# Optimization experiments

Measured on AMD Instinct MI355X. Metric: run time of the kernel, lower is better.

The kernel has to match this reference:

```python
import jax, jax.numpy as jnp
import numpy as np

B, G = 64, 48            # events, grid side -> N = B*G*G nodes
N = B * G * G
DIMS = [128, 102, 73, 44, 16]   # channel schedule from GraphZ defaults
KERN = 3                 # GMM kernels on the conv layer
MAXV = 1.0               # Cartesian(max_value=neighbors=1)


def _build_graph():
    # 3x3 window graph (radius 1, self loops) per event, as in window_edges
    ix, iy = np.meshgrid(np.arange(G), np.arange(G), indexing='ij')
    ix, iy = ix.ravel(), iy.ravel()
    srcs, tgts = [], []
    for dx in (-1, 0, 1):
        for dy in (-1, 0, 1):
            jx, jy = ix + dx, iy + dy
            m = (jx >= 0) & (jx < G) & (jy >= 0) & (jy < G)
            srcs.append(jx[m] * G + jy[m])
            tgts.append(ix[m] * G + iy[m])
    src, tgt = np.concatenate(srcs), np.concatenate(tgts)
    base = (np.arange(B) * G * G)[:, None]
    ei = np.stack([(base + src[None]).ravel(), (base + tgt[None]).ravel()])
    pos = np.stack([np.tile(ix, B).astype(np.float32),
                    np.tile(iy, B).astype(np.float32),
                    np.repeat(np.arange(B), G * G).astype(np.float32)], axis=1)
    return ei.astype(np.int32), pos


def setup_inputs() -> dict:
    key = jax.random.key(0)
    ks = jax.random.split(key, 16)
    ei, pos = _build_graph()
    inp = {
        'x': jax.random.normal(ks[0], (N, DIMS[0]), jnp.float32),
        'pos': jnp.asarray(pos),
        'edge_index': jnp.asarray(ei),
    }
    # pointwise layer 0: 128->102 (+BN)
    inp['w0'] = jax.random.normal(ks[1], (DIMS[0], DIMS[1]), jnp.float32) * (1.0 / np.sqrt(DIMS[0]))
    inp['b0'] = jnp.zeros((DIMS[1],), jnp.float32)
    inp['gamma0'] = jnp.ones((DIMS[1],), jnp.float32)
    inp['beta0'] = jnp.zeros((DIMS[1],), jnp.float32)
    # pointwise layer 1: 102->73 (+BN)
    inp['w1'] = jax.random.normal(ks[2], (DIMS[1], DIMS[2]), jnp.float32) * (1.0 / np.sqrt(DIMS[1]))
    inp['b1'] = jnp.zeros((DIMS[2],), jnp.float32)
    inp['gamma1'] = jnp.ones((DIMS[2],), jnp.float32)
    inp['beta1'] = jnp.zeros((DIMS[2],), jnp.float32)
    # GMM conv layer 2: 73->44, 3 gaussian kernels (+BN)
    inp['w2'] = jax.random.normal(ks[3], (DIMS[2], DIMS[3]), jnp.float32) * (1.0 / np.sqrt(DIMS[2]))
    inp['g2'] = jax.random.normal(ks[4], (DIMS[2], KERN * DIMS[3]), jnp.float32) * (1.0 / np.sqrt(DIMS[2]))
    inp['mu2'] = jax.random.uniform(ks[5], (KERN, 2), jnp.float32)
    inp['sigma2'] = jax.random.uniform(ks[6], (KERN, 2), jnp.float32) + 0.5
    inp['b2'] = jnp.zeros((DIMS[3],), jnp.float32)
    inp['gamma2'] = jnp.ones((DIMS[3],), jnp.float32)
    inp['beta2'] = jnp.zeros((DIMS[3],), jnp.float32)
    # pointwise layer 3: 44->16
    inp['w3'] = jax.random.normal(ks[7], (DIMS[3], DIMS[4]), jnp.float32) * (1.0 / np.sqrt(DIMS[3]))
    inp['b3'] = jnp.zeros((DIMS[4],), jnp.float32)
    return inp


def _bn(x, gamma, beta):
    # BatchNorm1d training forward: biased batch stats over the node dim
    m = jnp.mean(x, axis=0)
    v = jnp.mean((x - m) ** 2, axis=0)
    return (x - m) * jax.lax.rsqrt(v + 1e-5) * gamma + beta


def _gmm_conv(x, ei, ea, g, mu, sigma, w_root, b, n):
    # PyG GMMConv (separate_gaussians=False, aggr='mean', root_weight, bias)
    E = ea.shape[0]
    kk = mu.shape[0]
    out = w_root.shape[1]
    xj = (x @ g)[ei[0]].reshape(E, kk, out)                 # gather transformed src feats
    gauss = jnp.exp(jnp.sum(-0.5 * (ea[:, None, :] - mu[None]) ** 2
                            / (1e-15 + sigma[None] ** 2), axis=-1))  # [E, K]
    msg = jnp.einsum('eko,ek->eo', xj, gauss)               # [E, out]
    s = jax.ops.segment_sum(msg, ei[1], num_segments=n)     # scatter-add to targets
    c = jax.ops.segment_sum(jnp.ones((E,), x.dtype), ei[1], num_segments=n)
    return s / jnp.maximum(c, 1.0)[:, None] + x @ w_root + b


def reference(x, pos, edge_index, w0, b0, gamma0, beta0, w1, b1, gamma1, beta1,
              w2, g2, mu2, sigma2, b2, gamma2, beta2, w3, b3):
    n = x.shape[0]
    pos2 = pos[:, :2]
    # Cartesian(max_value=1, norm=True): pseudo coords in [0, 1]
    ea = (pos2[edge_index[0]] - pos2[edge_index[1]]) / (2.0 * MAXV) + 0.5
    # layers 0,1: knn_graph(k=0) -> empty edge set -> GMMConv = root Linear + bias
    h = _bn(x @ w0 + b0, gamma0, beta0)
    h = _bn(h @ w1 + b1, gamma1, beta1)
    # layer 2: window-edge GMMConv with 3 gaussian kernels
    h = _bn(_gmm_conv(h, edge_index, ea, g2, mu2, sigma2, w2, b2, n), gamma2, beta2)
    # layer 3: pointwise, no norm
    return h @ w3 + b3
```

## Files before the change

kernel.cpp:

```cpp
#include <hip/hip_runtime.h>

#define GRIDW 48
#define NNODES 147456
#define NTILES 2304
#define GB 512
#define NSH 8
#define SHS 128

typedef __attribute__((ext_vector_type(8))) short short8;
typedef __attribute__((ext_vector_type(4))) float f32x4;

__device__ inline unsigned short f2bf(float f) {
    union { float f; unsigned u; } v; v.f = f;
    unsigned r = v.u + 0x7FFFu + ((v.u >> 16) & 1u);
    return (unsigned short)(r >> 16);
}
__device__ inline float bf2f(unsigned short h) {
    union { unsigned u; float f; } v; v.u = ((unsigned)h) << 16;
    return v.f;
}

__global__ void prep(const float* __restrict__ w0, const float* __restrict__ b0,
                     const float* __restrict__ w1, const float* __restrict__ b1,
                     const float* __restrict__ g2, const float* __restrict__ w2,
                     const float* __restrict__ b2, const float* __restrict__ w3,
                     const float* __restrict__ b3,
                     unsigned short* __restrict__ wt0, unsigned short* __restrict__ wt1,
                     unsigned short* __restrict__ wt2, unsigned short* __restrict__ wt3,
                     float* __restrict__ biasf0, float* __restrict__ biasf1,
                     float* __restrict__ biasf2, float* __restrict__ biasf3,
                     float* __restrict__ statz) {
    int id = blockIdx.x * 256 + threadIdx.x;
    if (id < 14336) {
        int col = id >> 7, k = id & 127;
        wt0[id] = (col < 102) ? f2bf(w0[k * 102 + col]) : (unsigned short)0;
    } else if (id < 24576) {
        int e = id - 14336; int col = e >> 7, k = e & 127;
        wt1[e] = (col < 73 && k < 102) ? f2bf(w1[k * 73 + col]) : (unsigned short)0;
    } else if (id < 41472) {
        int e = id - 24576; int col = e / 96, k = e - (e / 96) * 96;
        unsigned short v = 0;
        if (k < 73) v = (col < 132) ? f2bf(g2[k * 132 + col]) : f2bf(w2[k * 44 + (col - 132)]);
        wt2[e] = v;
    } else if (id < 42496) {
        int e = id - 41472; int col = e >> 6, k = e & 63;
        wt3[e] = (k < 44) ? f2bf(w3[k * 16 + col]) : (unsigned short)0;
    } else if (id < 42608) { int c = id - 42496; biasf0[c] = (c < 102) ? b0[c] : 0.f; }
    else if (id < 42688) { int c = id - 42608; biasf1[c] = (c < 73) ? b1[c] : 0.f; }
    else if (id < 42864) { int c = id - 42688; biasf2[c] = (c < 132) ? 0.f : b2[c - 132]; }
    else if (id < 42880) { int c = id - 42864; biasf3[c] = b3[c]; }
    else if (id < 49024) { statz[id - 42880] = 0.f; }
}

template<int K, int KP, int MP, int MOUT, int PREVM, int BNSRC,
         bool STATS, bool OUTBF, bool ABF16>
__global__ __launch_bounds__(256) void gemm_p(
    const void* __restrict__ Ain, const unsigned short* __restrict__ WT,
    const float* __restrict__ biasf,
    const float* __restrict__ q0, const float* __restrict__ q1,
    const float* __restrict__ q2, const float* __restrict__ q3,
    float invN, void* __restrict__ Yout,
    float* __restrict__ sumO, float* __restrict__ ssO)
{
    constexpr int KS = KP + 8;
    constexpr int NCF = MP / 16;
    constexpr int UPR = ABF16 ? (K / 8) : (K / 4);
    constexpr int TOT = 64 * UPR;
    constexpr int NLD = (TOT + 255) / 256;
    __shared__ __align__(16) unsigned short As[2][64 * KS];
    __shared__ __align__(16) unsigned short Bs[MP * KS];
    __shared__ float bnA[KP], bnB[KP];

    const int tid = threadIdx.x;
    const int lane = tid & 63, wv = tid >> 6, qd = lane >> 4, lc = lane & 15;

    if (BNSRC == 1) {
        if (tid < KP) {
            float a = 0.f, b = 0.f;
            if (tid < PREVM) {
                float s0 = 0.f, s1 = 0.f;
#pragma unroll
                for (int sh = 0; sh < NSH; ++sh) {
                    s0 += q0[sh * SHS + tid];
                    s1 += q1[sh * SHS + tid];
                }
                float m = s0 * invN;
                float v = s1 * invN - m * m;
                float sc = q2[tid] * rsqrtf(v + 1e-5f);
                a = sc; b = q3[tid] - m * sc;
            }
            bnA[tid] = a; bnB[tid] = b;
        }
    }
    for (int g = tid; g < MP * (KP / 8); g += 256) {
        int col = g / (KP / 8), u = g - col * (KP / 8);
        *(uint4*)&Bs[col * KS + u * 8] = *(const uint4*)&WT[(size_t)col * KP + u * 8];
    }
    if constexpr (KP > K) {
        constexpr int PADU = (KP - K) / 2;
        for (int g = tid; g < 64 * PADU; g += 256) {
            int row = g / PADU, u = g - row * PADU;
            *(unsigned*)&As[0][row * KS + K + u * 2] = 0u;
            *(unsigned*)&As[1][row * KS + K + u * 2] = 0u;
        }
    }

    float bvr[NCF];
#pragma unroll
    for (int cf = 0; cf < NCF; ++cf) bvr[cf] = biasf[cf * 16 + lc];

    float cs[NCF], cq[NCF];
    if (STATS) {
#pragma unroll
        for (int cf = 0; cf < NCF; ++cf) { cs[cf] = 0.f; cq[cf] = 0.f; }
    }

    uint4 pfb[NLD];
    float4 pff[NLD];

    int t = blockIdx.x;
#pragma unroll
    for (int i = 0; i < NLD; ++i) {
        int g = tid + 256 * i;
        if (g < TOT) {
            if constexpr (ABF16)
                pfb[i] = *(const uint4*)((const unsigned short*)Ain + (size_t)t * 64 * K + g * 8);
            else
                pff[i] = *(const float4*)((const float*)Ain + (size_t)t * 64 * K + g * 4);
        }
    }
    __syncthreads();

    int buf = 0;
    for (; t < NTILES; t += GB) {
#pragma unroll
        for (int i = 0; i < NLD; ++i) {
            int g = tid + 256 * i;
            if (g < TOT) {
                int row = g / UPR, u = g - row * UPR;
                if constexpr (ABF16) {
                    uint4 w = pfb[i];
                    if (BNSRC != 0) {
                        unsigned* wp = (unsigned*)&w;
#pragma unroll
                        for (int pp = 0; pp < 4; ++pp) {
                            int kk = u * 8 + 2 * pp;
                            float lo = bf2f((unsigned short)(wp[pp] & 0xFFFFu)) * bnA[kk] + bnB[kk];
                            float hi = bf2f((unsigned short)(wp[pp] >> 16)) * bnA[kk + 1] + bnB[kk + 1];
                            wp[pp] = (unsigned)f2bf(lo) | ((unsigned)f2bf(hi) << 16);
                        }
                    }
                    *(uint4*)&As[buf][row * KS + u * 8] = w;
                } else {
                    float4 v = pff[i];
                    if (BNSRC != 0) {
                        int kk = u * 4;
                        v.x = v.x * bnA[kk] + bnB[kk];
                        v.y = v.y * bnA[kk + 1] + bnB[kk + 1];
                        v.z = v.z * bnA[kk + 2] + bnB[kk + 2];
                        v.w = v.w * bnA[kk + 3] + bnB[kk + 3];
                    }
                    unsigned lo = (unsigned)f2bf(v.x) | ((unsigned)f2bf(v.y) << 16);
                    unsigned hi = (unsigned)f2bf(v.z) | ((unsigned)f2bf(v.w) << 16);
                    *(uint2*)&As[buf][row * KS + u * 4] = make_uint2(lo, hi);
                }
            }
        }
        int t2 = t + GB;
        if (t2 < NTILES) {
#pragma unroll
            for (int i = 0; i < NLD; ++i) {
                int g = tid + 256 * i;
                if (g < TOT) {
                    if constexpr (ABF16)
                        pfb[i] = *(const uint4*)((const unsigned short*)Ain + (size_t)t2 * 64 * K + g * 8);
                    else
                        pff[i] = *(const float4*)((const float*)Ain + (size_t)t2 * 64 * K + g * 4);
                }
            }
        }
        __syncthreads();

        f32x4 acc[NCF];
#pragma unroll
        for (int cf = 0; cf < NCF; ++cf) acc[cf] = (f32x4){0.f, 0.f, 0.f, 0.f};
#pragma unroll
        for (int kt = 0; kt < KP / 32; ++kt) {
            const int kb = kt * 32 + qd * 8;
            short8 a = *(const short8*)&As[buf][(wv * 16 + lc) * KS + kb];
#pragma unroll
            for (int cf = 0; cf < NCF; ++cf) {
                short8 b = *(const short8*)&Bs[(cf * 16 + lc) * KS + kb];
                acc[cf] = __builtin_amdgcn_mfma_f32_16x16x32_bf16(a, b, acc[cf], 0, 0, 0);
            }
        }
#pragma unroll
        for (int cf = 0; cf < NCF; ++cf) {
            const int col = cf * 16 + lc;
            const float bv = bvr[cf];
#pragma unroll
            for (int rr = 0; rr < 4; ++rr) {
                float v = acc[cf][rr] + bv;
                int row = t * 64 + wv * 16 + qd * 4 + rr;
                if (OUTBF) ((unsigned short*)Yout)[(size_t)row * MP + col] = f2bf(v);
                else       ((float*)Yout)[(size_t)row * MP + col] = v;
                if (STATS) { cs[cf] += v; cq[cf] += v * v; }
            }
        }
        buf ^= 1;
    }

    if (STATS) {
        __syncthreads();
        float* red = (float*)As;
        float* redq = red + 4 * MP;
#pragma unroll
        for (int cf = 0; cf < NCF; ++cf) {
            float s = cs[cf], qq = cq[cf];
            s += __shfl_down(s, 32, 64); s += __shfl_down(s, 16, 64);
            qq += __shfl_down(qq, 32, 64); qq += __shfl_down(qq, 16, 64);
            if (lane < 16) {
                red[wv * MP + cf * 16 + lane] = s;
                redq[wv * MP + cf * 16 + lane] = qq;
            }
        }
        __syncthreads();
        if (tid < MOUT) {
            float s = red[tid] + red[MP + tid] + red[2 * MP + tid] + red[3 * MP + tid];
            float qq = redq[tid] + redq[MP + tid] + redq[2 * MP + tid] + redq[3 * MP + tid];
            const int sh = blockIdx.x & (NSH - 1);
            atomicAdd(&sumO[sh * SHS + tid], s);
            atomicAdd(&ssO[sh * SHS + tid], qq);
        }
    }
}

__device__ __forceinline__ void load_u(const unsigned short* __restrict__ TR,
                                       int b, int jx, int iy, int c0,
                                       const float (*gy)[3], float (&u)[12]) {
#pragma unroll
    for (int j = 0; j < 12; ++j) u[j] = 0.f;
    if (jx < 0 || jx >= GRIDW) return;
    const unsigned short* rowp = TR + (size_t)(b * 2304 + jx * 48) * 176;
#pragma unroll
    for (int dy = -1; dy <= 1; ++dy) {
        int jy = iy + dy;
        if (jy < 0 || jy >= GRIDW) continue;
        const unsigned short* np = rowp + (size_t)jy * 176 + c0;
#pragma unroll
        for (int k = 0; k < 3; ++k) {
            uint2 v = *(const uint2*)(np + k * 44);
            float g = gy[dy + 1][k];
            u[k * 4 + 0] += g * bf2f((unsigned short)(v.x & 0xFFFFu));
            u[k * 4 + 1] += g * bf2f((unsigned short)(v.x >> 16));
            u[k * 4 + 2] += g * bf2f((unsigned short)(v.y & 0xFFFFu));
            u[k * 4 + 3] += g * bf2f((unsigned short)(v.y >> 16));
        }
    }
}

__global__ __launch_bounds__(256) void gmm_stencil(
    const unsigned short* __restrict__ TR, unsigned short* __restrict__ C,
    const float* __restrict__ mu, const float* __restrict__ sigma,
    float* __restrict__ sum2, float* __restrict__ ss2)
{
    __shared__ float gx[3][3], gy[3][3];
    __shared__ float red[88];
    const int tid = threadIdx.x;
    if (tid < 88) red[tid] = 0.f;
    if (tid < 18) {
        int d = (tid / 3) % 3, k = tid % 3;
        bool isy = tid >= 9;
        float e = 0.5f * (float)(d - 1) + 0.5f;
        float mm = mu[k * 2 + (isy ? 1 : 0)];
        float sg = sigma[k * 2 + (isy ? 1 : 0)];
        float v = expf(-0.5f * (e - mm) * (e - mm) / (1e-15f + sg * sg));
        if (isy) gy[d][k] = v; else gx[d][k] = v;
    }
    __syncthreads();

    const int xcd = blockIdx.x & 7;
    const int bi  = blockIdx.x >> 3;
    const int b   = xcd * 8 + bi / 33;
    const unsigned tau = (unsigned)(bi % 33) * 256u + (unsigned)tid;
    const int og = (int)(tau % 11u);
    const unsigned r1 = tau / 11u;
    const int iy = (int)(r1 % 48u);
    const int x0 = (int)(r1 / 48u) * 3;
    const int c0 = og * 4;

    float u0[12], u1[12], u2[12];
    load_u(TR, b, x0 - 1, iy, c0, gy, u0);
    load_u(TR, b, x0,     iy, c0, gy, u1);
    float s4[4] = {0, 0, 0, 0}, q4[4] = {0, 0, 0, 0};
    const int ny = 1 + (iy > 0) + (iy < GRIDW - 1);

#define GSTEP(ST, UA, UB, UC)                                                  \
    {                                                                          \
        const int ix = x0 + (ST);                                              \
        load_u(TR, b, ix + 1, iy, c0, gy, UC);                                 \
        const int nx = 1 + (ix > 0) + (ix < GRIDW - 1);                        \
        const float inv = 1.f / (float)(nx * ny);                              \
        const int node = b * 2304 + ix * 48 + iy;                              \
        uint2 rv = *(const uint2*)(TR + (size_t)node * 176 + 132 + c0);        \
        float o[4];                                                            \
        _Pragma("unroll")                                                      \
        for (int j = 0; j < 4; ++j) {                                          \
            float acc = 0.f;                                                   \
            _Pragma("unroll")                                                  \
            for (int k = 0; k < 3; ++k)                                        \
                acc += gx[0][k] * UA[k * 4 + j] + gx[1][k] * UB[k * 4 + j]     \
                     + gx[2][k] * UC[k * 4 + j];                               \
            o[j] = acc * inv;                                                  \
        }                                                                      \
        o[0] += bf2f((unsigned short)(rv.x & 0xFFFFu));                        \
        o[1] += bf2f((unsigned short)(rv.x >> 16));                            \
        o[2] += bf2f((unsigned short)(rv.y & 0xFFFFu));                        \
        o[3] += bf2f((unsigned short)(rv.y >> 16));                            \
        unsigned lo = (unsigned)f2bf(o[0]) | ((unsigned)f2bf(o[1]) << 16);     \
        unsigned hi = (unsigned)f2bf(o[2]) | ((unsigned)f2bf(o[3]) << 16);     \
        *(uint2*)&C[(size_t)node * 48 + c0] = make_uint2(lo, hi);              \
        if (og == 10)                                                          \
            *(uint2*)&C[(size_t)node * 48 + 44] = make_uint2(0u, 0u);          \
        _Pragma("unroll")                                                      \
        for (int j = 0; j < 4; ++j) { s4[j] += o[j]; q4[j] += o[j] * o[j]; }   \
    }

    GSTEP(0, u0, u1, u2)
    GSTEP(1, u1, u2, u0)
    GSTEP(2, u2, u0, u1)
#undef GSTEP

#pragma unroll
    for (int j = 0; j < 4; ++j) {
        atomicAdd(&red[c0 + j], s4[j]);
        atomicAdd(&red[44 + c0 + j], q4[j]);
    }
    __syncthreads();
    if (tid < 88) {
        const int sh = blockIdx.x & (NSH - 1);
        if (tid < 44) atomicAdd(&sum2[sh * SHS + tid], red[tid]);
        else          atomicAdd(&ss2[sh * SHS + tid - 44], red[tid]);
    }
}

extern "C" void kernel_launch(void* const* d_in, const int* in_sizes, int n_in,
                              void* d_out, int out_size, void* d_ws, size_t ws_size,
                              hipStream_t stream) {
    const float* x      = (const float*)d_in[0];
    const float* w0     = (const float*)d_in[3];
    const float* b0     = (const float*)d_in[4];
    const float* gamma0 = (const float*)d_in[5];
    const float* beta0  = (const float*)d_in[6];
    const float* w1     = (const float*)d_in[7];
    const float* b1     = (const float*)d_in[8];
    const float* gamma1 = (const float*)d_in[9];
    const float* beta1  = (const float*)d_in[10];
    const float* w2     = (const float*)d_in[11];
    const float* g2     = (const float*)d_in[12];
    const float* mu2    = (const float*)d_in[13];
    const float* sigma2 = (const float*)d_in[14];
    const float* b2     = (const float*)d_in[15];
    const float* gamma2 = (const float*)d_in[16];
    const float* beta2  = (const float*)d_in[17];
    const float* w3     = (const float*)d_in[18];
    const float* b3     = (const float*)d_in[19];
    float* out = (float*)d_out;

    const int N = NNODES;
    const float invN = 1.0f / (float)N;

    const size_t tailOff = (size_t)N * 132;
    size_t need = (tailOff + 300000) * sizeof(float);
    if (ws_size < need) return;

    float* ws = (float*)d_ws;
    unsigned short* bufY1 = (unsigned short*)ws;
    unsigned short* bufC  = (unsigned short*)ws;
    unsigned short* bufY0 = (unsigned short*)(ws + (size_t)N * 44);
    unsigned short* bufTR = bufY0;

    float* tail = ws + tailOff;
    float* sum0 = tail;
    float* ss0  = tail + 1024;
    float* sum1 = tail + 2048;
    float* ss1  = tail + 3072;
    float* sum2 = tail + 4096;
    float* ss2  = tail + 5120;
    float* biasf0 = tail + 6144;
    float* biasf1 = tail + 6256;
    float* biasf2 = tail + 6336;
    float* biasf3 = tail + 6512;
    unsigned short* wt0 = (unsigned short*)(tail + 6528);
    unsigned short* wt1 = wt0 + 14336;
    unsigned short* wt2 = wt1 + 10240;
    unsigned short* wt3 = wt2 + 16896;

    prep<<<192, 256, 0, stream>>>(w0, b0, w1, b1, g2, w2, b2, w3, b3,
                                  wt0, wt1, wt2, wt3,
                                  biasf0, biasf1, biasf2, biasf3, tail);

    gemm_p<128, 128, 112, 102, 0, 0, true, true, false><<<GB, 256, 0, stream>>>(
        x, wt0, biasf0, nullptr, nullptr, nullptr, nullptr, invN, bufY0, sum0, ss0);

    gemm_p<112, 128, 80, 73, 102, 1, true, true, true><<<GB, 256, 0, stream>>>(
        bufY0, wt1, biasf1, sum0, ss0, gamma0, beta0, invN, bufY1, sum1, ss1);

    gemm_p<80, 96, 176, 176, 73, 1, false, true, true><<<GB, 256, 0, stream>>>(
        bufY1, wt2, biasf2, sum1, ss1, gamma1, beta1, invN, bufTR, nullptr, nullptr);

    gmm_stencil<<<2112, 256, 0, stream>>>(bufTR, bufC, mu2, sigma2, sum2, ss2);

    gemm_p<48, 64, 16, 16, 44, 1, false, false, true><<<GB, 256, 0, stream>>>(
        bufC, wt3, biasf3, sum2, ss2, gamma2, beta2, invN, out, nullptr, nullptr);
}
```

Before: 240.9 us.

## Store GMM transform channel-major and restructure stencil to node-per-thread with LDS staging

The third GEMM now writes its 176-column bf16 output channel-major (planar per channel), and the stencil kernel is rewritten so each thread owns one node and loops over the 11 channel groups. It reads coalesced neighbour values from the planar layout, stages results in LDS, computes BN statistics from the tile, and writes row-major output with wide stores. This targets the strided 8-byte gathers of the old row-major stencil. In exchange it drops the register reuse of the sliding x-window, so each neighbour is reloaded per channel, and the GEMM epilogue's channel-major stores are scattered.

```diff
diff --git a/kernel.cpp b/kernel.cpp
--- a/kernel.cpp
+++ b/kernel.cpp
@@ -53,7 +53,7 @@
 }
 
 template<int K, int KP, int MP, int MOUT, int PREVM, int BNSRC,
-         bool STATS, bool OUTBF, bool ABF16>
+         bool STATS, bool OUTBF, bool ABF16, bool OUTCM>
 __global__ __launch_bounds__(256) void gemm_p(
     const void* __restrict__ Ain, const unsigned short* __restrict__ WT,
     const float* __restrict__ biasf,
@@ -198,13 +198,23 @@
         for (int cf = 0; cf < NCF; ++cf) {
             const int col = cf * 16 + lc;
             const float bv = bvr[cf];
-#pragma unroll
-            for (int rr = 0; rr < 4; ++rr) {
-                float v = acc[cf][rr] + bv;
-                int row = t * 64 + wv * 16 + qd * 4 + rr;
-                if (OUTBF) ((unsigned short*)Yout)[(size_t)row * MP + col] = f2bf(v);
-                else       ((float*)Yout)[(size_t)row * MP + col] = v;
-                if (STATS) { cs[cf] += v; cq[cf] += v * v; }
+            if constexpr (OUTCM) {
+                const int row0 = t * 64 + wv * 16 + qd * 4;
+                unsigned lo = (unsigned)f2bf(acc[cf][0] + bv)
+                            | ((unsigned)f2bf(acc[cf][1] + bv) << 16);
+                unsigned hi = (unsigned)f2bf(acc[cf][2] + bv)
+                            | ((unsigned)f2bf(acc[cf][3] + bv) << 16);
+                *(uint2*)((unsigned short*)Yout + (size_t)col * NNODES + row0) =
+                    make_uint2(lo, hi);
+            } else {
+#pragma unroll
+                for (int rr = 0; rr < 4; ++rr) {
+                    float v = acc[cf][rr] + bv;
+                    int row = t * 64 + wv * 16 + qd * 4 + rr;
+                    if (OUTBF) ((unsigned short*)Yout)[(size_t)row * MP + col] = f2bf(v);
+                    else       ((float*)Yout)[(size_t)row * MP + col] = v;
+                    if (STATS) { cs[cf] += v; cq[cf] += v * v; }
+                }
             }
         }
         buf ^= 1;
@@ -235,36 +245,14 @@
     }
 }
 
-__device__ __forceinline__ void load_u(const unsigned short* __restrict__ TR,
-                                       int b, int jx, int iy, int c0,
-                                       const float (*gy)[3], float (&u)[12]) {
-#pragma unroll
-    for (int j = 0; j < 12; ++j) u[j] = 0.f;
-    if (jx < 0 || jx >= GRIDW) return;
-    const unsigned short* rowp = TR + (size_t)(b * 2304 + jx * 48) * 176;
-#pragma unroll
-    for (int dy = -1; dy <= 1; ++dy) {
-        int jy = iy + dy;
-        if (jy < 0 || jy >= GRIDW) continue;
-        const unsigned short* np = rowp + (size_t)jy * 176 + c0;
-#pragma unroll
-        for (int k = 0; k < 3; ++k) {
-            uint2 v = *(const uint2*)(np + k * 44);
-            float g = gy[dy + 1][k];
-            u[k * 4 + 0] += g * bf2f((unsigned short)(v.x & 0xFFFFu));
-            u[k * 4 + 1] += g * bf2f((unsigned short)(v.x >> 16));
-            u[k * 4 + 2] += g * bf2f((unsigned short)(v.y & 0xFFFFu));
-            u[k * 4 + 3] += g * bf2f((unsigned short)(v.y >> 16));
-        }
-    }
-}
-
 __global__ __launch_bounds__(256) void gmm_stencil(
-    const unsigned short* __restrict__ TR, unsigned short* __restrict__ C,
+    const unsigned short* __restrict__ TR2, unsigned short* __restrict__ C,
     const float* __restrict__ mu, const float* __restrict__ sigma,
     float* __restrict__ sum2, float* __restrict__ ss2)
 {
-    __shared__ float gx[3][3], gy[3][3];
+    constexpr int CT = 56;
+    __shared__ __align__(16) unsigned short Ctile[256 * CT];
+    __shared__ float gxs[3][3], gys[3][3];
     __shared__ float red[88];
     const int tid = threadIdx.x;
     if (tid < 88) red[tid] = 0.f;
@@ -275,70 +263,104 @@
         float mm = mu[k * 2 + (isy ? 1 : 0)];
         float sg = sigma[k * 2 + (isy ? 1 : 0)];
         float v = expf(-0.5f * (e - mm) * (e - mm) / (1e-15f + sg * sg));
-        if (isy) gy[d][k] = v; else gx[d][k] = v;
+        if (isy) gys[d][k] = v; else gxs[d][k] = v;
     }
     __syncthreads();
 
-    const int xcd = blockIdx.x & 7;
-    const int bi  = blockIdx.x >> 3;
-    const int b   = xcd * 8 + bi / 33;
-    const unsigned tau = (unsigned)(bi % 33) * 256u + (unsigned)tid;
-    const int og = (int)(tau % 11u);
-    const unsigned r1 = tau / 11u;
-    const int iy = (int)(r1 % 48u);
-    const int x0 = (int)(r1 / 48u) * 3;
-    const int c0 = og * 4;
-
-    float u0[12], u1[12], u2[12];
-    load_u(TR, b, x0 - 1, iy, c0, gy, u0);
-    load_u(TR, b, x0,     iy, c0, gy, u1);
-    float s4[4] = {0, 0, 0, 0}, q4[4] = {0, 0, 0, 0};
+    const int wg = blockIdx.x;
+    const int gb = (wg & 7) * 72 + (wg >> 3);
+    const int node0 = gb << 8;
+    const int node = node0 + tid;
+    const int iy  = node % 48;
+    const int ixg = (node / 48) % 48;
+
+    const int eym = (iy > 0) ? 1 : 0;
+    const int eyp = (iy < GRIDW - 1) ? 1 : 0;
+    const float my0 = (iy > 0) ? 1.f : 0.f;
+    const float my2 = (iy < GRIDW - 1) ? 1.f : 0.f;
+    const int dxm = (ixg > 0) ? 48 : 0;
+    const int dxp = (ixg < GRIDW - 1) ? 48 : 0;
+    const float wxm = (ixg > 0) ? 1.f : 0.f;
+    const float wxp = (ixg < GRIDW - 1) ? 1.f : 0.f;
+    const int nx = 1 + (ixg > 0) + (ixg < GRIDW - 1);
     const int ny = 1 + (iy > 0) + (iy < GRIDW - 1);
-
-#define GSTEP(ST, UA, UB, UC)                                                  \
-    {                                                                          \
-        const int ix = x0 + (ST);                                              \
-        load_u(TR, b, ix + 1, iy, c0, gy, UC);                                 \
-        const int nx = 1 + (ix > 0) + (ix < GRIDW - 1);                        \
-        const float inv = 1.f / (float)(nx * ny);                              \
-        const int node = b * 2304 + ix * 48 + iy;                              \
-        uint2 rv = *(const uint2*)(TR + (size_t)node * 176 + 132 + c0);        \
-        float o[4];                                                            \
-        _Pragma("unroll")                                                      \
-        for (int j = 0; j < 4; ++j) {                                          \
-            float acc = 0.f;                                                   \
+    const float inv = 1.f / (float)(nx * ny);
+
+    float gxr[3][3], wym[3], wyc[3], wyp[3];
+#pragma unroll
+    for (int k = 0; k < 3; ++k) {
+        gxr[0][k] = gxs[0][k]; gxr[1][k] = gxs[1][k]; gxr[2][k] = gxs[2][k];
+        wym[k] = my0 * gys[0][k];
+        wyc[k] = gys[1][k];
+        wyp[k] = my2 * gys[2][k];
+    }
+
+#pragma unroll 1
+    for (int og = 0; og < 11; ++og) {
+        const int c0 = og * 4;
+        const size_t pb = (size_t)c0 * NNODES;
+        f32x4 o = (f32x4){0.f, 0.f, 0.f, 0.f};
+
+#define COLU(U, CB, WX)                                                        \
+        f32x4 U;                                                               \
+        {                                                                      \
+            const int cb_ = (CB);                                              \
             _Pragma("unroll")                                                  \
-            for (int k = 0; k < 3; ++k)                                        \
-                acc += gx[0][k] * UA[k * 4 + j] + gx[1][k] * UB[k * 4 + j]     \
-                     + gx[2][k] * UC[k * 4 + j];                               \
-            o[j] = acc * inv;                                                  \
-        }                                                                      \
-        o[0] += bf2f((unsigned short)(rv.x & 0xFFFFu));                        \
-        o[1] += bf2f((unsigned short)(rv.x >> 16));                            \
-        o[2] += bf2f((unsigned short)(rv.y & 0xFFFFu));                        \
-        o[3] += bf2f((unsigned short)(rv.y >> 16));                            \
-        unsigned lo = (unsigned)f2bf(o[0]) | ((unsigned)f2bf(o[1]) << 16);     \
-        unsigned hi = (unsigned)f2bf(o[2]) | ((unsigned)f2bf(o[3]) << 16);     \
-        *(uint2*)&C[(size_t)node * 48 + c0] = make_uint2(lo, hi);              \
-        if (og == 10)                                                          \
-            *(uint2*)&C[(size_t)node * 48 + 44] = make_uint2(0u, 0u);          \
-        _Pragma("unroll")                                                      \
-        for (int j = 0; j < 4; ++j) { s4[j] += o[j]; q4[j] += o[j] * o[j]; }   \
-    }
-
-    GSTEP(0, u0, u1, u2)
-    GSTEP(1, u1, u2, u0)
-    GSTEP(2, u2, u0, u1)
-#undef GSTEP
-
-#pragma unroll
-    for (int j = 0; j < 4; ++j) {
-        atomicAdd(&red[c0 + j], s4[j]);
-        atomicAdd(&red[44 + c0 + j], q4[j]);
+            for (int j = 0; j < 4; ++j) {                                      \
+                const unsigned short* pl =                                     \
+                    TR2 + pb + (size_t)(k * 44 + j) * NNODES;                  \
+                float vm = bf2f(pl[cb_ - eym]);                                \
+                float vc = bf2f(pl[cb_]);                                      \
+                float vp = bf2f(pl[cb_ + eyp]);                                \
+                U[j] = ((WX) * wym[k]) * vm + ((WX) * wyc[k]) * vc             \
+                     + ((WX) * wyp[k]) * vp;                                   \
+            }                                                                  \
+        }
+
+#pragma unroll
+        for (int k = 0; k < 3; ++k) {
+            COLU(uL, node - dxm, wxm)
+            COLU(uC, node,       1.f)
+            COLU(uR, node + dxp, wxp)
+            o += gxr[0][k] * uL + gxr[1][k] * uC + gxr[2][k] * uR;
+        }
+#undef COLU
+
+        o = o * inv;
+        const unsigned short* rp = TR2 + (size_t)(132 + c0) * NNODES;
+        o.x += bf2f(rp[node]);
+        o.y += bf2f(rp[NNODES + node]);
+        o.z += bf2f(rp[2 * (size_t)NNODES + node]);
+        o.w += bf2f(rp[3 * (size_t)NNODES + node]);
+
+        unsigned lo = (unsigned)f2bf(o.x) | ((unsigned)f2bf(o.y) << 16);
+        unsigned hi = (unsigned)f2bf(o.z) | ((unsigned)f2bf(o.w) << 16);
+        *(uint2*)&Ctile[tid * CT + c0] = make_uint2(lo, hi);
+    }
+    *(uint2*)&Ctile[tid * CT + 44] = make_uint2(0u, 0u);
+    __syncthreads();
+
+    {
+        const int lane = tid & 63, w4 = tid >> 6;
+        if (lane < 44) {
+            float s = 0.f, q = 0.f;
+            const int nb = w4 * 64;
+            for (int n = nb; n < nb + 64; ++n) {
+                float v = bf2f(Ctile[n * CT + lane]);
+                s += v; q += v * v;
+            }
+            atomicAdd(&red[lane], s);
+            atomicAdd(&red[44 + lane], q);
+        }
+    }
+    for (int g = tid; g < 1536; g += 256) {
+        int n = g / 6, part = g - n * 6;
+        *(uint4*)&C[(size_t)(node0 + n) * 48 + part * 8] =
+            *(const uint4*)&Ctile[n * CT + part * 8];
     }
     __syncthreads();
     if (tid < 88) {
-        const int sh = blockIdx.x & (NSH - 1);
+        const int sh = wg & (NSH - 1);
         if (tid < 44) atomicAdd(&sum2[sh * SHS + tid], red[tid]);
         else          atomicAdd(&ss2[sh * SHS + tid - 44], red[tid]);
     }
@@ -400,17 +422,17 @@
                                   wt0, wt1, wt2, wt3,
                                   biasf0, biasf1, biasf2, biasf3, tail);
 
-    gemm_p<128, 128, 112, 102, 0, 0, true, true, false><<<GB, 256, 0, stream>>>(
+    gemm_p<128, 128, 112, 102, 0, 0, true, true, false, false><<<GB, 256, 0, stream>>>(
         x, wt0, biasf0, nullptr, nullptr, nullptr, nullptr, invN, bufY0, sum0, ss0);
 
-    gemm_p<112, 128, 80, 73, 102, 1, true, true, true><<<GB, 256, 0, stream>>>(
+    gemm_p<112, 128, 80, 73, 102, 1, true, true, true, false><<<GB, 256, 0, stream>>>(
         bufY0, wt1, biasf1, sum0, ss0, gamma0, beta0, invN, bufY1, sum1, ss1);
 
-    gemm_p<80, 96, 176, 176, 73, 1, false, true, true><<<GB, 256, 0, stream>>>(
+    gemm_p<80, 96, 176, 176, 73, 1, false, true, true, true><<<GB, 256, 0, stream>>>(
         bufY1, wt2, biasf2, sum1, ss1, gamma1, beta1, invN, bufTR, nullptr, nullptr);
 
-    gmm_stencil<<<2112, 256, 0, stream>>>(bufTR, bufC, mu2, sigma2, sum2, ss2);
-
-    gemm_p<48, 64, 16, 16, 44, 1, false, false, true><<<GB, 256, 0, stream>>>(
+    gmm_stencil<<<576, 256, 0, stream>>>(bufTR, bufC, mu2, sigma2, sum2, ss2);
+
+    gemm_p<48, 64, 16, 16, 44, 1, false, false, true, false><<<GB, 256, 0, stream>>>(
         bufC, wt3, biasf3, sum2, ss2, gamma2, beta2, invN, out, nullptr, nullptr);
 }
```

Measured after the change: 333.9 us. 38.6% more time.

## Stage GEMM A tiles via global_load_lds and fold BatchNorm into weights

Applied to the files above, without the earlier changes.

Replaces the register-prefetch and convert-to-LDS staging of A tiles with direct global-to-LDS async loads (global_load_lds, 16 bytes per lane) in a k-block-major layout. fp32 input is kept in LDS and converted to bf16 at fragment-load time. BatchNorm of the previous layer is folded into the weight columns and an output bias, so the per-element affine on activations is dropped. This aims to remove VGPR pressure and VALU work in the load path, at the cost of an extra barrier per tile, a larger fp32 LDS buffer, and bf16 rounding of the scaled weights.

```diff
diff --git a/kernel.cpp b/kernel.cpp
--- a/kernel.cpp
+++ b/kernel.cpp
@@ -19,6 +19,11 @@
     union { unsigned u; float f; } v; v.u = ((unsigned)h) << 16;
     return v.f;
 }
+
+#define GL2LDS16(g, l)                                                         \
+    __builtin_amdgcn_global_load_lds(                                          \
+        (const __attribute__((address_space(1))) unsigned int*)(g),            \
+        (__attribute__((address_space(3))) unsigned int*)(l), 16, 0, 0)
 
 __global__ void prep(const float* __restrict__ w0, const float* __restrict__ b0,
                      const float* __restrict__ w1, const float* __restrict__ b1,
@@ -53,7 +58,7 @@
 }
 
 template<int K, int KP, int MP, int MOUT, int PREVM, int BNSRC,
-         bool STATS, bool OUTBF, bool ABF16>
+         bool STATS, bool OUTBF, bool AF32>
 __global__ __launch_bounds__(256) void gemm_p(
     const void* __restrict__ Ain, const unsigned short* __restrict__ WT,
     const float* __restrict__ biasf,
@@ -62,14 +67,15 @@
     float invN, void* __restrict__ Yout,
     float* __restrict__ sumO, float* __restrict__ ssO)
 {
-    constexpr int KS = KP + 8;
-    constexpr int NCF = MP / 16;
-    constexpr int UPR = ABF16 ? (K / 8) : (K / 4);
-    constexpr int TOT = 64 * UPR;
-    constexpr int NLD = (TOT + 255) / 256;
-    __shared__ __align__(16) unsigned short As[2][64 * KS];
-    __shared__ __align__(16) unsigned short Bs[MP * KS];
-    __shared__ float bnA[KP], bnB[KP];
+    constexpr int KBLK = K / 8;
+    constexpr int KBP  = KP / 8;
+    constexpr int ABUF = AF32 ? (KP * 64 * 4) : (KP * 64 * 2);
+    constexpr int BS_S = KP + 8;
+    constexpr int NCF  = MP / 16;
+
+    __shared__ __align__(16) unsigned char Abuf[2][ABUF];
+    __shared__ __align__(16) unsigned short Bs[MP * BS_S];
+    __shared__ float bnA[KP], bnB[KP], outb[MP];
 
     const int tid = threadIdx.x;
     const int lane = tid & 63, wv = tid >> 6, qd = lane >> 4, lc = lane & 15;
@@ -91,23 +97,57 @@
             }
             bnA[tid] = a; bnB[tid] = b;
         }
-    }
+        if (tid < MP) outb[tid] = 0.f;
+    }
+    if constexpr (!AF32 && KP > K) {
+        constexpr int PADU = (KBP - KBLK) * 256;
+        for (int g = tid; g < PADU; g += 256) {
+            ((unsigned int*)&Abuf[0][KBLK * 1024])[g] = 0u;
+            ((unsigned int*)&Abuf[1][KBLK * 1024])[g] = 0u;
+        }
+    }
+    __syncthreads();
+
     for (int g = tid; g < MP * (KP / 8); g += 256) {
         int col = g / (KP / 8), u = g - col * (KP / 8);
-        *(uint4*)&Bs[col * KS + u * 8] = *(const uint4*)&WT[(size_t)col * KP + u * 8];
-    }
-    if constexpr (KP > K) {
-        constexpr int PADU = (KP - K) / 2;
-        for (int g = tid; g < 64 * PADU; g += 256) {
-            int row = g / PADU, u = g - row * PADU;
-            *(unsigned*)&As[0][row * KS + K + u * 2] = 0u;
-            *(unsigned*)&As[1][row * KS + K + u * 2] = 0u;
-        }
-    }
+        uint4 w = *(const uint4*)&WT[(size_t)col * KP + u * 8];
+        if (BNSRC == 1) {
+            unsigned* wp = (unsigned*)&w;
+            float ob = 0.f;
+#pragma unroll
+            for (int pp = 0; pp < 4; ++pp) {
+                int kk = u * 8 + 2 * pp;
+                float lo = bf2f((unsigned short)(wp[pp] & 0xFFFFu));
+                float hi = bf2f((unsigned short)(wp[pp] >> 16));
+                ob += lo * bnB[kk] + hi * bnB[kk + 1];
+                lo *= bnA[kk]; hi *= bnA[kk + 1];
+                wp[pp] = (unsigned)f2bf(lo) | ((unsigned)f2bf(hi) << 16);
+            }
+            atomicAdd(&outb[col], ob);
+        }
+        *(uint4*)&Bs[col * BS_S + u * 8] = w;
+    }
+
+    auto STAGE = [&](int t, int bb) {
+        if constexpr (AF32) {
+            const float* src = (const float*)Ain + (size_t)t * 64 * K;
+            for (int i = wv; i < K / 4; i += 4)
+                GL2LDS16(src + (size_t)lane * K + i * 4, &Abuf[bb][i * 1024]);
+        } else {
+            const unsigned short* src =
+                (const unsigned short*)Ain + (size_t)t * 64 * K;
+            for (int i = wv; i < K / 8; i += 4)
+                GL2LDS16(src + (size_t)lane * K + i * 8, &Abuf[bb][i * 1024]);
+        }
+    };
+
+    STAGE(blockIdx.x, 0);
+    __syncthreads();
 
     float bvr[NCF];
 #pragma unroll
-    for (int cf = 0; cf < NCF; ++cf) bvr[cf] = biasf[cf * 16 + lc];
+    for (int cf = 0; cf < NCF; ++cf)
+        bvr[cf] = biasf[cf * 16 + lc] + (BNSRC == 1 ? outb[cf * 16 + lc] : 0.f);
 
     float cs[NCF], cq[NCF];
     if (STATS) {
@@ -115,82 +155,34 @@
         for (int cf = 0; cf < NCF; ++cf) { cs[cf] = 0.f; cq[cf] = 0.f; }
     }
 
-    uint4 pfb[NLD];
-    float4 pff[NLD];
-
-    int t = blockIdx.x;
-#pragma unroll
-    for (int i = 0; i < NLD; ++i) {
-        int g = tid + 256 * i;
-        if (g < TOT) {
-            if constexpr (ABF16)
-                pfb[i] = *(const uint4*)((const unsigned short*)Ain + (size_t)t * 64 * K + g * 8);
-            else
-                pff[i] = *(const float4*)((const float*)Ain + (size_t)t * 64 * K + g * 4);
-        }
-    }
-    __syncthreads();
-
+    const int row = wv * 16 + lc;
     int buf = 0;
-    for (; t < NTILES; t += GB) {
-#pragma unroll
-        for (int i = 0; i < NLD; ++i) {
-            int g = tid + 256 * i;
-            if (g < TOT) {
-                int row = g / UPR, u = g - row * UPR;
-                if constexpr (ABF16) {
-                    uint4 w = pfb[i];
-                    if (BNSRC != 0) {
-                        unsigned* wp = (unsigned*)&w;
-#pragma unroll
-                        for (int pp = 0; pp < 4; ++pp) {
-                            int kk = u * 8 + 2 * pp;
-                            float lo = bf2f((unsigned short)(wp[pp] & 0xFFFFu)) * bnA[kk] + bnB[kk];
-                            float hi = bf2f((unsigned short)(wp[pp] >> 16)) * bnA[kk + 1] + bnB[kk + 1];
-                            wp[pp] = (unsigned)f2bf(lo) | ((unsigned)f2bf(hi) << 16);
-                        }
-                    }
-                    *(uint4*)&As[buf][row * KS + u * 8] = w;
-                } else {
-                    float4 v = pff[i];
-                    if (BNSRC != 0) {
-                        int kk = u * 4;
-                        v.x = v.x * bnA[kk] + bnB[kk];
-                        v.y = v.y * bnA[kk + 1] + bnB[kk + 1];
-                        v.z = v.z * bnA[kk + 2] + bnB[kk + 2];
-                        v.w = v.w * bnA[kk + 3] + bnB[kk + 3];
-                    }
-                    unsigned lo = (unsigned)f2bf(v.x) | ((unsigned)f2bf(v.y) << 16);
-                    unsigned hi = (unsigned)f2bf(v.z) | ((unsigned)f2bf(v.w) << 16);
-                    *(uint2*)&As[buf][row * KS + u * 4] = make_uint2(lo, hi);
-                }
-            }
-        }
-        int t2 = t + GB;
-        if (t2 < NTILES) {
-#pragma unroll
-            for (int i = 0; i < NLD; ++i) {
-                int g = tid + 256 * i;
-                if (g < TOT) {
-                    if constexpr (ABF16)
-                        pfb[i] = *(const uint4*)((const unsigned short*)Ain + (size_t)t2 * 64 * K + g * 8);
-                    else
-                        pff[i] = *(const float4*)((const float*)Ain + (size_t)t2 * 64 * K + g * 4);
-                }
-            }
-        }
-        __syncthreads();
+    for (int t = blockIdx.x; t < NTILES; t += GB) {
+        const int t2 = t + GB;
+        if (t2 < NTILES) STAGE(t2, buf ^ 1);
 
         f32x4 acc[NCF];
 #pragma unroll
         for (int cf = 0; cf < NCF; ++cf) acc[cf] = (f32x4){0.f, 0.f, 0.f, 0.f};
 #pragma unroll
         for (int kt = 0; kt < KP / 32; ++kt) {
-            const int kb = kt * 32 + qd * 8;
-            short8 a = *(const short8*)&As[buf][(wv * 16 + lc) * KS + kb];
+            short8 a;
+            if constexpr (AF32) {
+                const int k4 = kt * 8 + qd * 2;
+                const float* Af = (const float*)&Abuf[buf][0];
+                float4 v0 = *(const float4*)&Af[(k4 * 64 + row) * 4];
+                float4 v1 = *(const float4*)&Af[((k4 + 1) * 64 + row) * 4];
+                a[0] = (short)f2bf(v0.x); a[1] = (short)f2bf(v0.y);
+                a[2] = (short)f2bf(v0.z); a[3] = (short)f2bf(v0.w);
+                a[4] = (short)f2bf(v1.x); a[5] = (short)f2bf(v1.y);
+                a[6] = (short)f2bf(v1.z); a[7] = (short)f2bf(v1.w);
+            } else {
+                const int kblock = kt * 4 + qd;
+                a = *(const short8*)&Abuf[buf][(kblock * 64 + row) * 16];
+            }
 #pragma unroll
             for (int cf = 0; cf < NCF; ++cf) {
-                short8 b = *(const short8*)&Bs[(cf * 16 + lc) * KS + kb];
+                short8 b = *(const short8*)&Bs[(cf * 16 + lc) * BS_S + kt * 32 + qd * 8];
                 acc[cf] = __builtin_amdgcn_mfma_f32_16x16x32_bf16(a, b, acc[cf], 0, 0, 0);
             }
         }
@@ -201,18 +193,19 @@
 #pragma unroll
             for (int rr = 0; rr < 4; ++rr) {
                 float v = acc[cf][rr] + bv;
-                int row = t * 64 + wv * 16 + qd * 4 + rr;
-                if (OUTBF) ((unsigned short*)Yout)[(size_t)row * MP + col] = f2bf(v);
-                else       ((float*)Yout)[(size_t)row * MP + col] = v;
+                int orow = t * 64 + wv * 16 + qd * 4 + rr;
+                if (OUTBF) ((unsigned short*)Yout)[(size_t)orow * MP + col] = f2bf(v);
+                else       ((float*)Yout)[(size_t)orow * MP + col] = v;
                 if (STATS) { cs[cf] += v; cq[cf] += v * v; }
             }
         }
+        __syncthreads();
         buf ^= 1;
     }
 
     if (STATS) {
         __syncthreads();
-        float* red = (float*)As;
+        float* red = (float*)Abuf;
         float* redq = red + 4 * MP;
 #pragma unroll
         for (int cf = 0; cf < NCF; ++cf) {
@@ -400,17 +393,17 @@
                                   wt0, wt1, wt2, wt3,
                                   biasf0, biasf1, biasf2, biasf3, tail);
 
-    gemm_p<128, 128, 112, 102, 0, 0, true, true, false><<<GB, 256, 0, stream>>>(
+    gemm_p<128, 128, 112, 102, 0, 0, true, true, true><<<GB, 256, 0, stream>>>(
         x, wt0, biasf0, nullptr, nullptr, nullptr, nullptr, invN, bufY0, sum0, ss0);
 
-    gemm_p<112, 128, 80, 73, 102, 1, true, true, true><<<GB, 256, 0, stream>>>(
+    gemm_p<112, 128, 80, 73, 102, 1, true, true, false><<<GB, 256, 0, stream>>>(
         bufY0, wt1, biasf1, sum0, ss0, gamma0, beta0, invN, bufY1, sum1, ss1);
 
-    gemm_p<80, 96, 176, 176, 73, 1, false, true, true><<<GB, 256, 0, stream>>>(
+    gemm_p<80, 96, 176, 176, 73, 1, false, true, false><<<GB, 256, 0, stream>>>(
         bufY1, wt2, biasf2, sum1, ss1, gamma1, beta1, invN, bufTR, nullptr, nullptr);
 
     gmm_stencil<<<2112, 256, 0, stream>>>(bufTR, bufC, mu2, sigma2, sum2, ss2);
 
-    gemm_p<48, 64, 16, 16, 44, 1, false, false, true><<<GB, 256, 0, stream>>>(
+    gemm_p<48, 64, 16, 16, 44, 1, false, false, false><<<GB, 256, 0, stream>>>(
         bufC, wt3, biasf3, sum2, ss2, gamma2, beta2, invN, out, nullptr, nullptr);
 }
```

Result: slower. 258.0 us (+7.1%).
